# Optimization experiments

Measured on AMD Instinct MI355X. Metric: run time of the kernel, lower is better.

The kernel has to match this reference:

```python
import jax, jax.numpy as jnp
import numpy as np

HEADS = 8
DIM_HEAD = 64
QUERY_DIM = 512
CONTEXT_DIM = 768
INNER = HEADS * DIM_HEAD  # 512
SCALE = DIM_HEAD ** -0.5


def setup_inputs() -> dict:
    key = jax.random.key(0)
    ks = jax.random.split(key, 7)
    B, N, M = 4, 2048, 2048
    x = jax.random.normal(ks[0], (B, N, QUERY_DIM), dtype=jnp.float32)
    context = jax.random.normal(ks[1], (B, M, CONTEXT_DIM), dtype=jnp.float32)
    # torch Linear weights: [out_features, in_features], y = x @ W.T
    s = 0.02
    Wq = jax.random.normal(ks[2], (INNER, QUERY_DIM), dtype=jnp.float32) * s
    Wk = jax.random.normal(ks[3], (INNER, CONTEXT_DIM), dtype=jnp.float32) * s
    Wv = jax.random.normal(ks[4], (INNER, CONTEXT_DIM), dtype=jnp.float32) * s
    Wo = jax.random.normal(ks[5], (QUERY_DIM, INNER), dtype=jnp.float32) * s
    bo = jax.random.normal(ks[6], (QUERY_DIM,), dtype=jnp.float32) * s
    return {"x": x, "context": context, "Wq": Wq, "Wk": Wk, "Wv": Wv, "Wo": Wo, "bo": bo}


def reference(x, context, Wq, Wk, Wv, Wo, bo):
    b, n, _ = x.shape
    m = context.shape[1]
    h, d = HEADS, DIM_HEAD
    # Projections (bias=False for q/k/v)
    q = jnp.einsum('bnc,ec->bne', x, Wq)        # [b, n, inner]
    k = jnp.einsum('bmc,ec->bme', context, Wk)  # [b, m, inner]
    v = jnp.einsum('bmc,ec->bme', context, Wv)
    # Split heads
    q = q.reshape(b, n, h, d)
    k = k.reshape(b, m, h, d)
    v = v.reshape(b, m, h, d)
    # Scores in fp32 (original casts q,k to float), scaled by dim_head**-0.5
    sim = jnp.einsum('bihd,bjhd->bhij', q.astype(jnp.float32), k.astype(jnp.float32)) * SCALE
    attn = jax.nn.softmax(sim, axis=-1).astype(v.dtype)
    out = jnp.einsum('bhij,bjhd->bihd', attn, v).reshape(b, n, h * d)
    # Output projection with bias (dropout=0 -> identity)
    return jnp.einsum('bne,oe->bno', out, Wo) + bo
```

## Files before the change

### kernel.cpp

```cpp
#include <hip/hip_runtime.h>
#include <hip/hip_bf16.h>
#include <math.h>


typedef __bf16 bf16x8 __attribute__((ext_vector_type(8)));
typedef __bf16 bf16x4 __attribute__((ext_vector_type(4)));
typedef short s16x4 __attribute__((ext_vector_type(4)));
typedef float f32x4 __attribute__((ext_vector_type(4)));

#define QSCALE 0.18033688011112042f

__device__ __forceinline__ f32x4 mfma32(bf16x8 a, bf16x8 b, f32x4 c) {
  return __builtin_amdgcn_mfma_f32_16x16x32_bf16(a, b, c, 0, 0, 0);
}
__device__ __forceinline__ f32x4 mfma16(s16x4 a, s16x4 b, f32x4 c) {
  return __builtin_amdgcn_mfma_f32_16x16x16bf16_1k(a, b, c, 0, 0, 0);
}

__global__ __launch_bounds__(256) void cast_all(
    const float* __restrict__ x, const float* __restrict__ ctx,
    const float* __restrict__ wq, const float* __restrict__ wk,
    const float* __restrict__ wv, const float* __restrict__ wo,
    __bf16* __restrict__ xb, __bf16* __restrict__ cb,
    __bf16* __restrict__ wqb, __bf16* __restrict__ wkb,
    __bf16* __restrict__ wvb, __bf16* __restrict__ wob) {
  const int B0 = 1048576;
  const int B1 = 2621440;
  const int B2 = 2686976;
  const int B3 = 2785280;
  const int B4 = 2883584;
  const int B5 = 2949120;
  for (int i = blockIdx.x * blockDim.x + threadIdx.x; i < B5;
       i += gridDim.x * blockDim.x) {
    const float* s;
    __bf16* d;
    int off;
    if (i < B0)      { s = x;   d = xb;  off = i; }
    else if (i < B1) { s = ctx; d = cb;  off = i - B0; }
    else if (i < B2) { s = wq;  d = wqb; off = i - B1; }
    else if (i < B3) { s = wk;  d = wkb; off = i - B2; }
    else if (i < B4) { s = wv;  d = wvb; off = i - B3; }
    else             { s = wo;  d = wob; off = i - B4; }
    float4 f = ((const float4*)s)[off];
    union { __bf16 b[4]; ushort4 u; } cv;
    cv.b[0] = (__bf16)f.x; cv.b[1] = (__bf16)f.y;
    cv.b[2] = (__bf16)f.z; cv.b[3] = (__bf16)f.w;
    ((ushort4*)d)[off] = cv.u;
  }
}

template <int MODE>
__device__ __forceinline__ void gemm_body(
    const __bf16* __restrict__ A, const __bf16* __restrict__ B,
    __bf16* __restrict__ Cout, int Kd, float scale, int m0, int n0,
    __bf16 (*As)[40], __bf16 (*Bs)[40]) {
  const int t = threadIdx.x;
  const int w = t >> 6;
  const int lane = t & 63;
  const int ln = lane & 15;
  const int qd = lane >> 4;
  const int wm = (w >> 1) * 64;
  const int wn = (w & 1) * 64;

  f32x4 zero4 = {0.f, 0.f, 0.f, 0.f};
  f32x4 acc[4][4];
#pragma unroll
  for (int i = 0; i < 4; ++i)
#pragma unroll
    for (int j = 0; j < 4; ++j) acc[i][j] = zero4;

  const int r = t >> 1;
  const int c0 = (t & 1) * 16;
  const __bf16* gA = A + (size_t)(m0 + r) * Kd + c0;
  const __bf16* gB = B + (size_t)(n0 + r) * Kd + c0;

  for (int kc = 0; kc < Kd; kc += 32) {
    uint4 a0 = *(const uint4*)(gA + kc);
    uint4 a1 = *(const uint4*)(gA + kc + 8);
    uint4 b0 = *(const uint4*)(gB + kc);
    uint4 b1 = *(const uint4*)(gB + kc + 8);
    __syncthreads();
    *(uint4*)&As[r][c0] = a0;
    *(uint4*)&As[r][c0 + 8] = a1;
    *(uint4*)&Bs[r][c0] = b0;
    *(uint4*)&Bs[r][c0 + 8] = b1;
    __syncthreads();
    bf16x8 af[4], bfr[4];
#pragma unroll
    for (int i = 0; i < 4; ++i) {
      af[i] = *(const bf16x8*)&As[wm + i * 16 + ln][qd * 8];
      bfr[i] = *(const bf16x8*)&Bs[wn + i * 16 + ln][qd * 8];
    }
#pragma unroll
    for (int i = 0; i < 4; ++i)
#pragma unroll
      for (int j = 0; j < 4; ++j) {
        if (MODE == 1)
          acc[i][j] = mfma32(af[i], bfr[j], acc[i][j]);
        else
          acc[i][j] = mfma32(bfr[j], af[i], acc[i][j]);
      }
  }

#pragma unroll
  for (int i = 0; i < 4; ++i)
#pragma unroll
    for (int j = 0; j < 4; ++j) {
      if (MODE == 0) {
        const int gm = m0 + wm + i * 16 + ln;
        const int gn0 = n0 + wn + j * 16 + qd * 4;
        const int bb = gm >> 11, tok = gm & 2047;
        const int hh = gn0 >> 6, dd0 = gn0 & 63;
        bf16x4 v;
#pragma unroll
        for (int rg = 0; rg < 4; ++rg) v[rg] = (__bf16)(acc[i][j][rg] * scale);
        *(bf16x4*)(Cout + (((size_t)bb * 8 + hh) * 2048 + tok) * 64 + dd0) = v;
      } else {
        const int gm0 = m0 + wm + i * 16 + qd * 4;
        const int gn = n0 + wn + j * 16 + ln;
        const int bb = gm0 >> 11, tok0 = gm0 & 2047;
        const int hh = gn >> 6, dd = gn & 63;
        bf16x4 v;
#pragma unroll
        for (int rg = 0; rg < 4; ++rg) v[rg] = (__bf16)acc[i][j][rg];
        *(bf16x4*)(Cout + (((size_t)bb * 8 + hh) * 64 + dd) * 2048 + tok0) = v;
      }
    }
}

__global__ __launch_bounds__(256, 3) void proj_qkv(
    const __bf16* __restrict__ xb, const __bf16* __restrict__ cb,
    const __bf16* __restrict__ Wq, const __bf16* __restrict__ Wk,
    const __bf16* __restrict__ Wv, __bf16* __restrict__ Qw,
    __bf16* __restrict__ Kw, __bf16* __restrict__ Vtw) {
  __shared__ __bf16 As[128][40];
  __shared__ __bf16 Bs[128][40];
  const int m0 = blockIdx.x * 128;
  const int job = blockIdx.y >> 2;
  const int n0 = (blockIdx.y & 3) * 128;
  if (job == 0)
    gemm_body<0>(xb, Wq, Qw, 512, QSCALE, m0, n0, As, Bs);
  else if (job == 1)
    gemm_body<0>(cb, Wk, Kw, 768, 1.0f, m0, n0, As, Bs);
  else
    gemm_body<1>(cb, Wv, Vtw, 768, 1.0f, m0, n0, As, Bs);
}

__global__ __launch_bounds__(256) void gemm_out(
    const __bf16* __restrict__ A,
    const __bf16* __restrict__ B,
    float* __restrict__ C,
    const float* __restrict__ bias) {
  const int m0 = blockIdx.x * 64;
  const int n0 = blockIdx.y * 128;
  const int t = threadIdx.x;
  const int w = t >> 6;
  const int lane = t & 63;
  const int ln = lane & 15;
  const int qd = lane >> 4;
  const int wm = (w >> 1) * 32;
  const int wn = (w & 1) * 64;

  __shared__ __bf16 As[64][40];
  __shared__ __bf16 Bs[128][40];

  f32x4 zero4 = {0.f, 0.f, 0.f, 0.f};
  f32x4 acc[2][4];
#pragma unroll
  for (int i = 0; i < 2; ++i)
#pragma unroll
    for (int j = 0; j < 4; ++j) acc[i][j] = zero4;

  const int ra = t >> 2, ca = (t & 3) * 8;
  const int rb = t >> 1, cb = (t & 1) * 16;
  const __bf16* gA = A + (size_t)(m0 + ra) * 512 + ca;
  const __bf16* gB = B + (size_t)(n0 + rb) * 512 + cb;

  for (int kc = 0; kc < 512; kc += 32) {
    uint4 av = *(const uint4*)(gA + kc);
    uint4 b0 = *(const uint4*)(gB + kc);
    uint4 b1 = *(const uint4*)(gB + kc + 8);
    __syncthreads();
    *(uint4*)&As[ra][ca] = av;
    *(uint4*)&Bs[rb][cb] = b0;
    *(uint4*)&Bs[rb][cb + 8] = b1;
    __syncthreads();
    bf16x8 af[2], bfr[4];
#pragma unroll
    for (int i = 0; i < 2; ++i)
      af[i] = *(const bf16x8*)&As[wm + i * 16 + ln][qd * 8];
#pragma unroll
    for (int j = 0; j < 4; ++j)
      bfr[j] = *(const bf16x8*)&Bs[wn + j * 16 + ln][qd * 8];
#pragma unroll
    for (int i = 0; i < 2; ++i)
#pragma unroll
      for (int j = 0; j < 4; ++j)
        acc[i][j] = mfma32(bfr[j], af[i], acc[i][j]);
  }

#pragma unroll
  for (int i = 0; i < 2; ++i)
#pragma unroll
    for (int j = 0; j < 4; ++j) {
      const int gm = m0 + wm + i * 16 + ln;
      const int gn0 = n0 + wn + j * 16 + qd * 4;
      f32x4 bi = *(const f32x4*)&bias[gn0];
      f32x4 v = acc[i][j] + bi;
      *(f32x4*)&C[(size_t)gm * 512 + gn0] = v;
    }
}

__global__ __launch_bounds__(256, 3) void attn_kernel(
    const __bf16* __restrict__ Q,
    const __bf16* __restrict__ K,
    const __bf16* __restrict__ Vt,
    __bf16* __restrict__ O) {
  const int S = 2048;
  const int qt = blockIdx.x;
  const int bh = blockIdx.y;
  const int b = bh >> 3, h = bh & 7;
  const int t = threadIdx.x;
  const int w = t >> 6;
  const int lane = t & 63;
  const int ln = lane & 15;
  const int qd = lane >> 4;

  __shared__ __bf16 Qs[64][68];
  __shared__ __bf16 Ks[128][72];
  __shared__ __bf16 Vts[64][132];

  {
    const int r = t >> 2, c = (t & 3) * 16;
    const uint4* g =
        (const uint4*)(Q + ((size_t)bh * S + qt * 64 + r) * 64 + c);
    uint4 q0 = g[0], q1 = g[1];
    uint2* d = (uint2*)&Qs[r][c];
    d[0] = *(uint2*)&q0; d[1] = *((uint2*)&q0 + 1);
    d[2] = *(uint2*)&q1; d[3] = *((uint2*)&q1 + 1);
  }

  f32x4 zero4 = {0.f, 0.f, 0.f, 0.f};
  f32x4 o[4];
#pragma unroll
  for (int i = 0; i < 4; ++i) o[i] = zero4;
  float lrow = 0.f;

  const int kr = t >> 1, kc = (t & 1) * 32;
  const int vd = t >> 2, vc = (t & 3) * 32;

  for (int kt = 0; kt < 16; ++kt) {
    const uint4* gK =
        (const uint4*)(K + ((size_t)bh * S + kt * 128 + kr) * 64 + kc);
    const uint4* gV =
        (const uint4*)(Vt + ((size_t)bh * 64 + vd) * S + kt * 128 + vc);
    uint4 kv0 = gK[0], kv1 = gK[1], kv2 = gK[2], kv3 = gK[3];
    uint4 vv0 = gV[0], vv1 = gV[1], vv2 = gV[2], vv3 = gV[3];
    __syncthreads();
    {
      uint4* dK = (uint4*)&Ks[kr][kc];
      dK[0] = kv0; dK[1] = kv1; dK[2] = kv2; dK[3] = kv3;
      uint2* dV = (uint2*)&Vts[vd][vc];
      dV[0] = *(uint2*)&vv0; dV[1] = *((uint2*)&vv0 + 1);
      dV[2] = *(uint2*)&vv1; dV[3] = *((uint2*)&vv1 + 1);
      dV[4] = *(uint2*)&vv2; dV[5] = *((uint2*)&vv2 + 1);
      dV[6] = *(uint2*)&vv3; dV[7] = *((uint2*)&vv3 + 1);
    }
    __syncthreads();

    f32x4 s[8];
#pragma unroll
    for (int nt = 0; nt < 8; ++nt) s[nt] = zero4;
#pragma unroll
    for (int kst = 0; kst < 2; ++kst) {
      union { bf16x4 hh[2]; bf16x8 v; } u;
      u.hh[0] = *(const bf16x4*)&Qs[w * 16 + ln][kst * 32 + qd * 8];
      u.hh[1] = *(const bf16x4*)&Qs[w * 16 + ln][kst * 32 + qd * 8 + 4];
      bf16x8 bq = u.v;
#pragma unroll
      for (int nt = 0; nt < 8; ++nt) {
        bf16x8 ak = *(const bf16x8*)&Ks[nt * 16 + ln][kst * 32 + qd * 8];
        s[nt] = mfma32(ak, bq, s[nt]);
      }
    }

    {
      float rs = 0.f;
#pragma unroll
      for (int nt = 0; nt < 8; ++nt)
#pragma unroll
        for (int rg = 0; rg < 4; ++rg) {
          float p = exp2f(s[nt][rg]);
          s[nt][rg] = p;
          rs += p;
        }
      lrow += rs;
    }

#pragma unroll
    for (int nt = 0; nt < 8; ++nt) {
      bf16x4 c0;
#pragma unroll
      for (int rg = 0; rg < 4; ++rg) c0[rg] = (__bf16)s[nt][rg];
      s16x4 p0 = __builtin_bit_cast(s16x4, c0);
#pragma unroll
      for (int i = 0; i < 4; ++i) {
        bf16x4 av = *(const bf16x4*)&Vts[i * 16 + ln][nt * 16 + qd * 4];
        s16x4 a = __builtin_bit_cast(s16x4, av);
        o[i] = mfma16(a, p0, o[i]);
      }
    }
  }

  {
    float l = lrow;
    l += __shfl_xor(l, 16);
    l += __shfl_xor(l, 32);
    const float inv = 1.f / l;
    const int tok = qt * 64 + w * 16 + ln;
#pragma unroll
    for (int i = 0; i < 4; ++i) {
      bf16x4 v;
#pragma unroll
      for (int rg = 0; rg < 4; ++rg) v[rg] = (__bf16)(o[i][rg] * inv);
      const int col = h * 64 + i * 16 + qd * 4;
      *(bf16x4*)&O[((size_t)b * S + tok) * 512 + col] = v;
    }
  }
}

extern "C" void kernel_launch(void* const* d_in, const int* in_sizes, int n_in,
                              void* d_out, int out_size, void* d_ws,
                              size_t ws_size, hipStream_t stream) {
  const float* x = (const float*)d_in[0];
  const float* ctx = (const float*)d_in[1];
  const float* Wq = (const float*)d_in[2];
  const float* Wk = (const float*)d_in[3];
  const float* Wv = (const float*)d_in[4];
  const float* Wo = (const float*)d_in[5];
  const float* bo = (const float*)d_in[6];

  char* p = (char*)d_ws;
  __bf16* xb = (__bf16*)p;   p += (size_t)8192 * 512 * 2;
  __bf16* cb = (__bf16*)p;   p += (size_t)8192 * 768 * 2;
  __bf16* wqb = (__bf16*)p;  p += (size_t)512 * 512 * 2;
  __bf16* wkb = (__bf16*)p;  p += (size_t)512 * 768 * 2;
  __bf16* wvb = (__bf16*)p;  p += (size_t)512 * 768 * 2;
  __bf16* wob = (__bf16*)p;  p += (size_t)512 * 512 * 2;
  __bf16* Qw = (__bf16*)p;   p += (size_t)8192 * 512 * 2;
  __bf16* Kw = (__bf16*)p;   p += (size_t)8192 * 512 * 2;
  __bf16* Vtw = (__bf16*)p;  p += (size_t)8192 * 512 * 2;
  __bf16* Ow = (__bf16*)p;   p += (size_t)8192 * 512 * 2;

  cast_all<<<2880, 256, 0, stream>>>(x, ctx, Wq, Wk, Wv, Wo, xb, cb, wqb, wkb,
                                     wvb, wob);

  dim3 gp(64, 12);
  proj_qkv<<<gp, 256, 0, stream>>>(xb, cb, wqb, wkb, wvb, Qw, Kw, Vtw);

  dim3 ga(32, 32);
  attn_kernel<<<ga, 256, 0, stream>>>(Qw, Kw, Vtw, Ow);

  dim3 go(128, 4);
  gemm_out<<<go, 256, 0, stream>>>(Ow, wob, (float*)d_out, bo);
}
```

Before: 205.6 us.

## Split attention over KV halves, merge in output GEMM, use global_load_lds staging

The attention kernel now handles 128 query rows per block and splits the key range into two halves along a new grid dimension. Each half writes unnormalized partial outputs and row sums. The output GEMM sums the two partials and normalizes them while loading A, which is valid because no running max is subtracted. The QKV projection and output GEMMs also stage their B operands, and for QKV both A and B, through global_load_lds into a k-sliced LDS layout instead of register round trips. This trades extra workspace traffic for the partials against more parallel blocks and reuse of each K/V tile across more query rows.

```diff
diff --git a/kernel.cpp b/kernel.cpp
--- a/kernel.cpp
+++ b/kernel.cpp
@@ -15,6 +15,12 @@
 }
 __device__ __forceinline__ f32x4 mfma16(s16x4 a, s16x4 b, f32x4 c) {
   return __builtin_amdgcn_mfma_f32_16x16x16bf16_1k(a, b, c, 0, 0, 0);
+}
+
+__device__ __forceinline__ void glds16(const void* g, void* l) {
+  __builtin_amdgcn_global_load_lds(
+      (const __attribute__((address_space(1))) unsigned int*)g,
+      (__attribute__((address_space(3))) unsigned int*)l, 16, 0, 0);
 }
 
 __global__ __launch_bounds__(256) void cast_all(
@@ -50,10 +56,10 @@
 }
 
 template <int MODE>
-__device__ __forceinline__ void gemm_body(
+__device__ __forceinline__ void gemm_body_g(
     const __bf16* __restrict__ A, const __bf16* __restrict__ B,
     __bf16* __restrict__ Cout, int Kd, float scale, int m0, int n0,
-    __bf16 (*As)[40], __bf16 (*Bs)[40]) {
+    __bf16 (*As)[128][8], __bf16 (*Bs)[128][8]) {
   const int t = threadIdx.x;
   const int w = t >> 6;
   const int lane = t & 63;
@@ -69,27 +75,23 @@
 #pragma unroll
     for (int j = 0; j < 4; ++j) acc[i][j] = zero4;
 
-  const int r = t >> 1;
-  const int c0 = (t & 1) * 16;
-  const __bf16* gA = A + (size_t)(m0 + r) * Kd + c0;
-  const __bf16* gB = B + (size_t)(n0 + r) * Kd + c0;
+  const __bf16* gA0 = A + (size_t)(m0 + lane) * Kd + w * 8;
+  const __bf16* gA1 = A + (size_t)(m0 + 64 + lane) * Kd + w * 8;
+  const __bf16* gB0 = B + (size_t)(n0 + lane) * Kd + w * 8;
+  const __bf16* gB1 = B + (size_t)(n0 + 64 + lane) * Kd + w * 8;
 
   for (int kc = 0; kc < Kd; kc += 32) {
-    uint4 a0 = *(const uint4*)(gA + kc);
-    uint4 a1 = *(const uint4*)(gA + kc + 8);
-    uint4 b0 = *(const uint4*)(gB + kc);
-    uint4 b1 = *(const uint4*)(gB + kc + 8);
-    __syncthreads();
-    *(uint4*)&As[r][c0] = a0;
-    *(uint4*)&As[r][c0 + 8] = a1;
-    *(uint4*)&Bs[r][c0] = b0;
-    *(uint4*)&Bs[r][c0 + 8] = b1;
+    __syncthreads();
+    glds16(gA0 + kc, &As[w][0][0]);
+    glds16(gA1 + kc, &As[w][64][0]);
+    glds16(gB0 + kc, &Bs[w][0][0]);
+    glds16(gB1 + kc, &Bs[w][64][0]);
     __syncthreads();
     bf16x8 af[4], bfr[4];
 #pragma unroll
     for (int i = 0; i < 4; ++i) {
-      af[i] = *(const bf16x8*)&As[wm + i * 16 + ln][qd * 8];
-      bfr[i] = *(const bf16x8*)&Bs[wn + i * 16 + ln][qd * 8];
+      af[i] = *(const bf16x8*)&As[qd][wm + i * 16 + ln][0];
+      bfr[i] = *(const bf16x8*)&Bs[qd][wn + i * 16 + ln][0];
     }
 #pragma unroll
     for (int i = 0; i < 4; ++i)
@@ -133,21 +135,23 @@
     const __bf16* __restrict__ Wq, const __bf16* __restrict__ Wk,
     const __bf16* __restrict__ Wv, __bf16* __restrict__ Qw,
     __bf16* __restrict__ Kw, __bf16* __restrict__ Vtw) {
-  __shared__ __bf16 As[128][40];
-  __shared__ __bf16 Bs[128][40];
+  __shared__ __align__(16) __bf16 As[4][128][8];
+  __shared__ __align__(16) __bf16 Bs[4][128][8];
   const int m0 = blockIdx.x * 128;
   const int job = blockIdx.y >> 2;
   const int n0 = (blockIdx.y & 3) * 128;
   if (job == 0)
-    gemm_body<0>(xb, Wq, Qw, 512, QSCALE, m0, n0, As, Bs);
+    gemm_body_g<0>(xb, Wq, Qw, 512, QSCALE, m0, n0, As, Bs);
   else if (job == 1)
-    gemm_body<0>(cb, Wk, Kw, 768, 1.0f, m0, n0, As, Bs);
+    gemm_body_g<0>(cb, Wk, Kw, 768, 1.0f, m0, n0, As, Bs);
   else
-    gemm_body<1>(cb, Wv, Vtw, 768, 1.0f, m0, n0, As, Bs);
+    gemm_body_g<1>(cb, Wv, Vtw, 768, 1.0f, m0, n0, As, Bs);
 }
 
 __global__ __launch_bounds__(256) void gemm_out(
-    const __bf16* __restrict__ A,
+    const __bf16* __restrict__ O0,
+    const __bf16* __restrict__ O1,
+    const float* __restrict__ lbuf,
     const __bf16* __restrict__ B,
     float* __restrict__ C,
     const float* __restrict__ bias) {
@@ -161,8 +165,8 @@
   const int wm = (w >> 1) * 32;
   const int wn = (w & 1) * 64;
 
-  __shared__ __bf16 As[64][40];
-  __shared__ __bf16 Bs[128][40];
+  __shared__ __align__(16) __bf16 As[64][40];
+  __shared__ __align__(16) __bf16 Bs[4][128][8];
 
   f32x4 zero4 = {0.f, 0.f, 0.f, 0.f};
   f32x4 acc[2][4];
@@ -172,18 +176,27 @@
     for (int j = 0; j < 4; ++j) acc[i][j] = zero4;
 
   const int ra = t >> 2, ca = (t & 3) * 8;
-  const int rb = t >> 1, cb = (t & 1) * 16;
-  const __bf16* gA = A + (size_t)(m0 + ra) * 512 + ca;
-  const __bf16* gB = B + (size_t)(n0 + rb) * 512 + cb;
+  const int gm_s = m0 + ra;
+  const int bidx = gm_s >> 11, tok_s = gm_s & 2047;
+  const size_t aoff = (size_t)gm_s * 512 + ca;
+  const __bf16* gB0 = B + (size_t)(n0 + lane) * 512 + w * 8;
+  const __bf16* gB1 = B + (size_t)(n0 + 64 + lane) * 512 + w * 8;
 
   for (int kc = 0; kc < 512; kc += 32) {
-    uint4 av = *(const uint4*)(gA + kc);
-    uint4 b0 = *(const uint4*)(gB + kc);
-    uint4 b1 = *(const uint4*)(gB + kc + 8);
-    __syncthreads();
-    *(uint4*)&As[ra][ca] = av;
-    *(uint4*)&Bs[rb][cb] = b0;
-    *(uint4*)&Bs[rb][cb + 8] = b1;
+    const int hh = kc >> 6;
+    const float l0 = lbuf[((size_t)bidx * 8 + hh) * 2048 + tok_s];
+    const float l1 = lbuf[(size_t)65536 + ((size_t)bidx * 8 + hh) * 2048 + tok_s];
+    const float inv = 1.0f / (l0 + l1);
+    union { bf16x8 v; uint4 u; } u0, u1, r;
+    u0.u = *(const uint4*)(O0 + aoff + kc);
+    u1.u = *(const uint4*)(O1 + aoff + kc);
+#pragma unroll
+    for (int e = 0; e < 8; ++e)
+      r.v[e] = (__bf16)(((float)u0.v[e] + (float)u1.v[e]) * inv);
+    __syncthreads();
+    glds16(gB0 + kc, &Bs[w][0][0]);
+    glds16(gB1 + kc, &Bs[w][64][0]);
+    *(uint4*)&As[ra][ca] = r.u;
     __syncthreads();
     bf16x8 af[2], bfr[4];
 #pragma unroll
@@ -191,7 +204,7 @@
       af[i] = *(const bf16x8*)&As[wm + i * 16 + ln][qd * 8];
 #pragma unroll
     for (int j = 0; j < 4; ++j)
-      bfr[j] = *(const bf16x8*)&Bs[wn + j * 16 + ln][qd * 8];
+      bfr[j] = *(const bf16x8*)&Bs[qd][wn + j * 16 + ln][0];
 #pragma unroll
     for (int i = 0; i < 2; ++i)
 #pragma unroll
@@ -215,10 +228,12 @@
     const __bf16* __restrict__ Q,
     const __bf16* __restrict__ K,
     const __bf16* __restrict__ Vt,
-    __bf16* __restrict__ O) {
+    __bf16* __restrict__ Oh,
+    float* __restrict__ lbuf) {
   const int S = 2048;
   const int qt = blockIdx.x;
   const int bh = blockIdx.y;
+  const int sp = blockIdx.z;
   const int b = bh >> 3, h = bh & 7;
   const int t = threadIdx.x;
   const int w = t >> 6;
@@ -226,30 +241,35 @@
   const int ln = lane & 15;
   const int qd = lane >> 4;
 
-  __shared__ __bf16 Qs[64][68];
-  __shared__ __bf16 Ks[128][72];
-  __shared__ __bf16 Vts[64][132];
+  __shared__ __align__(16) __bf16 Qs[128][68];
+  __shared__ __align__(16) __bf16 Ks[128][72];
+  __shared__ __align__(16) __bf16 Vts[64][132];
 
   {
-    const int r = t >> 2, c = (t & 3) * 16;
+    const int r = t >> 1, c = (t & 1) * 32;
     const uint4* g =
-        (const uint4*)(Q + ((size_t)bh * S + qt * 64 + r) * 64 + c);
-    uint4 q0 = g[0], q1 = g[1];
+        (const uint4*)(Q + ((size_t)bh * S + qt * 128 + r) * 64 + c);
+    uint4 q0 = g[0], q1 = g[1], q2 = g[2], q3 = g[3];
     uint2* d = (uint2*)&Qs[r][c];
     d[0] = *(uint2*)&q0; d[1] = *((uint2*)&q0 + 1);
     d[2] = *(uint2*)&q1; d[3] = *((uint2*)&q1 + 1);
+    d[4] = *(uint2*)&q2; d[5] = *((uint2*)&q2 + 1);
+    d[6] = *(uint2*)&q3; d[7] = *((uint2*)&q3 + 1);
   }
 
   f32x4 zero4 = {0.f, 0.f, 0.f, 0.f};
-  f32x4 o[4];
-#pragma unroll
-  for (int i = 0; i < 4; ++i) o[i] = zero4;
-  float lrow = 0.f;
+  f32x4 o[2][4];
+#pragma unroll
+  for (int mt = 0; mt < 2; ++mt)
+#pragma unroll
+    for (int i = 0; i < 4; ++i) o[mt][i] = zero4;
+  float lrow[2] = {0.f, 0.f};
 
   const int kr = t >> 1, kc = (t & 1) * 32;
   const int vd = t >> 2, vc = (t & 3) * 32;
-
-  for (int kt = 0; kt < 16; ++kt) {
+  const int kt0 = sp * 8;
+
+  for (int kt = kt0; kt < kt0 + 8; ++kt) {
     const uint4* gK =
         (const uint4*)(K + ((size_t)bh * S + kt * 128 + kr) * 64 + kc);
     const uint4* gV =
@@ -268,63 +288,82 @@
     }
     __syncthreads();
 
-    f32x4 s[8];
-#pragma unroll
-    for (int nt = 0; nt < 8; ++nt) s[nt] = zero4;
+    f32x4 s[2][8];
+#pragma unroll
+    for (int mt = 0; mt < 2; ++mt)
+#pragma unroll
+      for (int nt = 0; nt < 8; ++nt) s[mt][nt] = zero4;
 #pragma unroll
     for (int kst = 0; kst < 2; ++kst) {
-      union { bf16x4 hh[2]; bf16x8 v; } u;
-      u.hh[0] = *(const bf16x4*)&Qs[w * 16 + ln][kst * 32 + qd * 8];
-      u.hh[1] = *(const bf16x4*)&Qs[w * 16 + ln][kst * 32 + qd * 8 + 4];
-      bf16x8 bq = u.v;
+      bf16x8 bq[2];
+#pragma unroll
+      for (int mt = 0; mt < 2; ++mt) {
+        union { bf16x4 hh[2]; bf16x8 v; } u;
+        u.hh[0] = *(const bf16x4*)&Qs[w * 32 + mt * 16 + ln][kst * 32 + qd * 8];
+        u.hh[1] =
+            *(const bf16x4*)&Qs[w * 32 + mt * 16 + ln][kst * 32 + qd * 8 + 4];
+        bq[mt] = u.v;
+      }
 #pragma unroll
       for (int nt = 0; nt < 8; ++nt) {
         bf16x8 ak = *(const bf16x8*)&Ks[nt * 16 + ln][kst * 32 + qd * 8];
-        s[nt] = mfma32(ak, bq, s[nt]);
-      }
-    }
-
-    {
+        s[0][nt] = mfma32(ak, bq[0], s[0][nt]);
+        s[1][nt] = mfma32(ak, bq[1], s[1][nt]);
+      }
+    }
+
+#pragma unroll
+    for (int mt = 0; mt < 2; ++mt) {
       float rs = 0.f;
 #pragma unroll
       for (int nt = 0; nt < 8; ++nt)
 #pragma unroll
         for (int rg = 0; rg < 4; ++rg) {
-          float p = exp2f(s[nt][rg]);
-          s[nt][rg] = p;
+          float p = exp2f(s[mt][nt][rg]);
+          s[mt][nt][rg] = p;
           rs += p;
         }
-      lrow += rs;
+      lrow[mt] += rs;
     }
 
 #pragma unroll
     for (int nt = 0; nt < 8; ++nt) {
-      bf16x4 c0;
-#pragma unroll
-      for (int rg = 0; rg < 4; ++rg) c0[rg] = (__bf16)s[nt][rg];
-      s16x4 p0 = __builtin_bit_cast(s16x4, c0);
+      s16x4 p0, p1;
+      {
+        bf16x4 c0, c1;
+#pragma unroll
+        for (int rg = 0; rg < 4; ++rg) {
+          c0[rg] = (__bf16)s[0][nt][rg];
+          c1[rg] = (__bf16)s[1][nt][rg];
+        }
+        p0 = __builtin_bit_cast(s16x4, c0);
+        p1 = __builtin_bit_cast(s16x4, c1);
+      }
 #pragma unroll
       for (int i = 0; i < 4; ++i) {
         bf16x4 av = *(const bf16x4*)&Vts[i * 16 + ln][nt * 16 + qd * 4];
         s16x4 a = __builtin_bit_cast(s16x4, av);
-        o[i] = mfma16(a, p0, o[i]);
-      }
-    }
-  }
-
-  {
-    float l = lrow;
+        o[0][i] = mfma16(a, p0, o[0][i]);
+        o[1][i] = mfma16(a, p1, o[1][i]);
+      }
+    }
+  }
+
+  __bf16* Osp = Oh + (size_t)sp * 8192 * 512;
+#pragma unroll
+  for (int mt = 0; mt < 2; ++mt) {
+    float l = lrow[mt];
     l += __shfl_xor(l, 16);
     l += __shfl_xor(l, 32);
-    const float inv = 1.f / l;
-    const int tok = qt * 64 + w * 16 + ln;
+    const int tok = qt * 128 + w * 32 + mt * 16 + ln;
+    if (qd == 0) lbuf[((size_t)sp * 32 + bh) * 2048 + tok] = l;
 #pragma unroll
     for (int i = 0; i < 4; ++i) {
       bf16x4 v;
 #pragma unroll
-      for (int rg = 0; rg < 4; ++rg) v[rg] = (__bf16)(o[i][rg] * inv);
+      for (int rg = 0; rg < 4; ++rg) v[rg] = (__bf16)o[mt][i][rg];
       const int col = h * 64 + i * 16 + qd * 4;
-      *(bf16x4*)&O[((size_t)b * S + tok) * 512 + col] = v;
+      *(bf16x4*)&Osp[((size_t)b * S + tok) * 512 + col] = v;
     }
   }
 }
@@ -350,7 +389,8 @@
   __bf16* Qw = (__bf16*)p;   p += (size_t)8192 * 512 * 2;
   __bf16* Kw = (__bf16*)p;   p += (size_t)8192 * 512 * 2;
   __bf16* Vtw = (__bf16*)p;  p += (size_t)8192 * 512 * 2;
-  __bf16* Ow = (__bf16*)p;   p += (size_t)8192 * 512 * 2;
+  __bf16* Oh = (__bf16*)p;   p += (size_t)2 * 8192 * 512 * 2;
+  float* lbuf = (float*)p;   p += (size_t)2 * 32 * 2048 * 4;
 
   cast_all<<<2880, 256, 0, stream>>>(x, ctx, Wq, Wk, Wv, Wo, xb, cb, wqb, wkb,
                                      wvb, wob);
@@ -358,9 +398,10 @@
   dim3 gp(64, 12);
   proj_qkv<<<gp, 256, 0, stream>>>(xb, cb, wqb, wkb, wvb, Qw, Kw, Vtw);
 
-  dim3 ga(32, 32);
-  attn_kernel<<<ga, 256, 0, stream>>>(Qw, Kw, Vtw, Ow);
+  dim3 ga(16, 32, 2);
+  attn_kernel<<<ga, 256, 0, stream>>>(Qw, Kw, Vtw, Oh, lbuf);
 
   dim3 go(128, 4);
-  gemm_out<<<go, 256, 0, stream>>>(Ow, wob, (float*)d_out, bo);
-}
+  gemm_out<<<go, 256, 0, stream>>>(Oh, Oh + (size_t)8192 * 512, lbuf, wob,
+                                   (float*)d_out, bo);
+}
```

Measured after the change: 217.1 us. 5.6% more time.

## Split attention over key range, merge partial outputs in output GEMM

Applied to the files above, without the earlier changes.

Attention now splits the key sequence into two halves across a third grid dimension. Each block handles 128 queries held in registers instead of 64 staged in shared memory, and writes unnormalized partial outputs plus row sums. The output-projection GEMM loads both partials, sums them, divides by the combined row sum and converts before the matmul. V^T storage is permuted so each thread fetches a 16-byte PV operand instead of two 8-byte ones. The merge is correct without a running max only because the scores are used without max subtraction. This doubles the O intermediate traffic and adds the l buffer in exchange for more reuse of K/V per block and wider loads.

```diff
diff --git a/kernel.cpp b/kernel.cpp
--- a/kernel.cpp
+++ b/kernel.cpp
@@ -118,12 +118,15 @@
       } else {
         const int gm0 = m0 + wm + i * 16 + qd * 4;
         const int gn = n0 + wn + j * 16 + ln;
-        const int bb = gm0 >> 11, tok0 = gm0 & 2047;
+        const int bb = gm0 >> 11;
+        const int tokbase = (gm0 & 2047) & ~31;
+        const int up = qd * 8 + (i & 1) * 4;
         const int hh = gn >> 6, dd = gn & 63;
         bf16x4 v;
 #pragma unroll
         for (int rg = 0; rg < 4; ++rg) v[rg] = (__bf16)acc[i][j][rg];
-        *(bf16x4*)(Cout + (((size_t)bb * 8 + hh) * 64 + dd) * 2048 + tok0) = v;
+        *(bf16x4*)(Cout + (((size_t)bb * 8 + hh) * 64 + dd) * 2048 + tokbase +
+                   up) = v;
       }
     }
 }
@@ -147,10 +150,10 @@
 }
 
 __global__ __launch_bounds__(256) void gemm_out(
-    const __bf16* __restrict__ A,
+    const __bf16* __restrict__ O0, const __bf16* __restrict__ O1,
+    const float* __restrict__ lbuf,
     const __bf16* __restrict__ B,
-    float* __restrict__ C,
-    const float* __restrict__ bias) {
+    float* __restrict__ C, const float* __restrict__ bias) {
   const int m0 = blockIdx.x * 64;
   const int n0 = blockIdx.y * 128;
   const int t = threadIdx.x;
@@ -173,15 +176,32 @@
 
   const int ra = t >> 2, ca = (t & 3) * 8;
   const int rb = t >> 1, cb = (t & 1) * 16;
-  const __bf16* gA = A + (size_t)(m0 + ra) * 512 + ca;
+  const int gm_s = m0 + ra;
+  const int bidx = gm_s >> 11, tok_s = gm_s & 2047;
+  const size_t aoff = (size_t)gm_s * 512 + ca;
   const __bf16* gB = B + (size_t)(n0 + rb) * 512 + cb;
 
+  float inv[8];
+#pragma unroll
+  for (int hh = 0; hh < 8; ++hh) {
+    const float l0 = lbuf[((size_t)bidx * 8 + hh) * 2048 + tok_s];
+    const float l1 = lbuf[65536 + ((size_t)bidx * 8 + hh) * 2048 + tok_s];
+    inv[hh] = 1.0f / (l0 + l1);
+  }
+
+#pragma unroll
   for (int kc = 0; kc < 512; kc += 32) {
-    uint4 av = *(const uint4*)(gA + kc);
+    const float iv = inv[kc >> 6];
+    union { bf16x8 v; uint4 u; } u0, u1, rr;
+    u0.u = *(const uint4*)(O0 + aoff + kc);
+    u1.u = *(const uint4*)(O1 + aoff + kc);
     uint4 b0 = *(const uint4*)(gB + kc);
     uint4 b1 = *(const uint4*)(gB + kc + 8);
-    __syncthreads();
-    *(uint4*)&As[ra][ca] = av;
+#pragma unroll
+    for (int e = 0; e < 8; ++e)
+      rr.v[e] = (__bf16)(((float)u0.v[e] + (float)u1.v[e]) * iv);
+    __syncthreads();
+    *(uint4*)&As[ra][ca] = rr.u;
     *(uint4*)&Bs[rb][cb] = b0;
     *(uint4*)&Bs[rb][cb + 8] = b1;
     __syncthreads();
@@ -211,14 +231,16 @@
     }
 }
 
-__global__ __launch_bounds__(256, 3) void attn_kernel(
+__global__ __launch_bounds__(256, 4) void attn_kernel(
     const __bf16* __restrict__ Q,
     const __bf16* __restrict__ K,
     const __bf16* __restrict__ Vt,
-    __bf16* __restrict__ O) {
+    __bf16* __restrict__ Oh,
+    float* __restrict__ lbuf) {
   const int S = 2048;
   const int qt = blockIdx.x;
   const int bh = blockIdx.y;
+  const int sp = blockIdx.z;
   const int b = bh >> 3, h = bh & 7;
   const int t = threadIdx.x;
   const int w = t >> 6;
@@ -226,30 +248,33 @@
   const int ln = lane & 15;
   const int qd = lane >> 4;
 
-  __shared__ __bf16 Qs[64][68];
-  __shared__ __bf16 Ks[128][72];
-  __shared__ __bf16 Vts[64][132];
-
+  __shared__ __align__(16) __bf16 Ks[128][72];
+  __shared__ __align__(16) __bf16 Vts[64][136];
+
+  bf16x8 bq[2][2];
   {
-    const int r = t >> 2, c = (t & 3) * 16;
-    const uint4* g =
-        (const uint4*)(Q + ((size_t)bh * S + qt * 64 + r) * 64 + c);
-    uint4 q0 = g[0], q1 = g[1];
-    uint2* d = (uint2*)&Qs[r][c];
-    d[0] = *(uint2*)&q0; d[1] = *((uint2*)&q0 + 1);
-    d[2] = *(uint2*)&q1; d[3] = *((uint2*)&q1 + 1);
+    const __bf16* qb =
+        Q + ((size_t)bh * S + qt * 128 + w * 32 + ln) * 64 + qd * 8;
+#pragma unroll
+    for (int mt = 0; mt < 2; ++mt)
+#pragma unroll
+      for (int kst = 0; kst < 2; ++kst)
+        bq[mt][kst] = *(const bf16x8*)(qb + mt * 1024 + kst * 32);
   }
 
   f32x4 zero4 = {0.f, 0.f, 0.f, 0.f};
-  f32x4 o[4];
-#pragma unroll
-  for (int i = 0; i < 4; ++i) o[i] = zero4;
-  float lrow = 0.f;
+  f32x4 o[2][4];
+#pragma unroll
+  for (int mt = 0; mt < 2; ++mt)
+#pragma unroll
+    for (int i = 0; i < 4; ++i) o[mt][i] = zero4;
+  float lrow[2] = {0.f, 0.f};
 
   const int kr = t >> 1, kc = (t & 1) * 32;
   const int vd = t >> 2, vc = (t & 3) * 32;
-
-  for (int kt = 0; kt < 16; ++kt) {
+  const int kt0 = sp * 8;
+
+  for (int kt = kt0; kt < kt0 + 8; ++kt) {
     const uint4* gK =
         (const uint4*)(K + ((size_t)bh * S + kt * 128 + kr) * 64 + kc);
     const uint4* gV =
@@ -260,71 +285,80 @@
     {
       uint4* dK = (uint4*)&Ks[kr][kc];
       dK[0] = kv0; dK[1] = kv1; dK[2] = kv2; dK[3] = kv3;
-      uint2* dV = (uint2*)&Vts[vd][vc];
-      dV[0] = *(uint2*)&vv0; dV[1] = *((uint2*)&vv0 + 1);
-      dV[2] = *(uint2*)&vv1; dV[3] = *((uint2*)&vv1 + 1);
-      dV[4] = *(uint2*)&vv2; dV[5] = *((uint2*)&vv2 + 1);
-      dV[6] = *(uint2*)&vv3; dV[7] = *((uint2*)&vv3 + 1);
-    }
-    __syncthreads();
-
-    f32x4 s[8];
-#pragma unroll
-    for (int nt = 0; nt < 8; ++nt) s[nt] = zero4;
-#pragma unroll
-    for (int kst = 0; kst < 2; ++kst) {
-      union { bf16x4 hh[2]; bf16x8 v; } u;
-      u.hh[0] = *(const bf16x4*)&Qs[w * 16 + ln][kst * 32 + qd * 8];
-      u.hh[1] = *(const bf16x4*)&Qs[w * 16 + ln][kst * 32 + qd * 8 + 4];
-      bf16x8 bq = u.v;
-#pragma unroll
-      for (int nt = 0; nt < 8; ++nt) {
-        bf16x8 ak = *(const bf16x8*)&Ks[nt * 16 + ln][kst * 32 + qd * 8];
-        s[nt] = mfma32(ak, bq, s[nt]);
+      uint4* dV = (uint4*)&Vts[vd][vc];
+      dV[0] = vv0; dV[1] = vv1; dV[2] = vv2; dV[3] = vv3;
+    }
+    __syncthreads();
+
+#pragma unroll
+    for (int c = 0; c < 4; ++c) {
+      bf16x8 av[4];
+#pragma unroll
+      for (int i = 0; i < 4; ++i)
+        av[i] = *(const bf16x8*)&Vts[i * 16 + ln][c * 32 + qd * 8];
+
+      f32x4 s[2][2];
+      s[0][0] = zero4; s[0][1] = zero4; s[1][0] = zero4; s[1][1] = zero4;
+#pragma unroll
+      for (int e = 0; e < 2; ++e) {
+        const int nt = c * 2 + e;
+#pragma unroll
+        for (int kst = 0; kst < 2; ++kst) {
+          bf16x8 ak = *(const bf16x8*)&Ks[nt * 16 + ln][kst * 32 + qd * 8];
+          s[e][0] = mfma32(ak, bq[0][kst], s[e][0]);
+          s[e][1] = mfma32(ak, bq[1][kst], s[e][1]);
+        }
       }
-    }
-
-    {
-      float rs = 0.f;
-#pragma unroll
-      for (int nt = 0; nt < 8; ++nt)
+#pragma unroll
+      for (int e = 0; e < 2; ++e)
+#pragma unroll
+        for (int mt = 0; mt < 2; ++mt) {
+          float rs = 0.f;
+#pragma unroll
+          for (int rg = 0; rg < 4; ++rg) {
+            float p = exp2f(s[e][mt][rg]);
+            s[e][mt][rg] = p;
+            rs += p;
+          }
+          lrow[mt] += rs;
+        }
+#pragma unroll
+      for (int e = 0; e < 2; ++e) {
+        bf16x4 c0, c1;
 #pragma unroll
         for (int rg = 0; rg < 4; ++rg) {
-          float p = exp2f(s[nt][rg]);
-          s[nt][rg] = p;
-          rs += p;
+          c0[rg] = (__bf16)s[e][0][rg];
+          c1[rg] = (__bf16)s[e][1][rg];
         }
-      lrow += rs;
-    }
-
-#pragma unroll
-    for (int nt = 0; nt < 8; ++nt) {
-      bf16x4 c0;
-#pragma unroll
-      for (int rg = 0; rg < 4; ++rg) c0[rg] = (__bf16)s[nt][rg];
-      s16x4 p0 = __builtin_bit_cast(s16x4, c0);
-#pragma unroll
-      for (int i = 0; i < 4; ++i) {
-        bf16x4 av = *(const bf16x4*)&Vts[i * 16 + ln][nt * 16 + qd * 4];
-        s16x4 a = __builtin_bit_cast(s16x4, av);
-        o[i] = mfma16(a, p0, o[i]);
+        s16x4 p0 = __builtin_bit_cast(s16x4, c0);
+        s16x4 p1 = __builtin_bit_cast(s16x4, c1);
+#pragma unroll
+        for (int i = 0; i < 4; ++i) {
+          union { bf16x8 v; bf16x4 hh[2]; } U;
+          U.v = av[i];
+          s16x4 a = __builtin_bit_cast(s16x4, U.hh[e]);
+          o[0][i] = mfma16(a, p0, o[0][i]);
+          o[1][i] = mfma16(a, p1, o[1][i]);
+        }
       }
     }
   }
 
-  {
-    float l = lrow;
+  __bf16* Osp = Oh + (size_t)sp * 8192 * 512;
+#pragma unroll
+  for (int mt = 0; mt < 2; ++mt) {
+    float l = lrow[mt];
     l += __shfl_xor(l, 16);
     l += __shfl_xor(l, 32);
-    const float inv = 1.f / l;
-    const int tok = qt * 64 + w * 16 + ln;
+    const int tok = qt * 128 + w * 32 + mt * 16 + ln;
+    if (qd == 0) lbuf[((size_t)sp * 32 + bh) * 2048 + tok] = l;
 #pragma unroll
     for (int i = 0; i < 4; ++i) {
       bf16x4 v;
 #pragma unroll
-      for (int rg = 0; rg < 4; ++rg) v[rg] = (__bf16)(o[i][rg] * inv);
+      for (int rg = 0; rg < 4; ++rg) v[rg] = (__bf16)o[mt][i][rg];
       const int col = h * 64 + i * 16 + qd * 4;
-      *(bf16x4*)&O[((size_t)b * S + tok) * 512 + col] = v;
+      *(bf16x4*)&Osp[((size_t)b * S + tok) * 512 + col] = v;
     }
   }
 }
@@ -350,7 +384,8 @@
   __bf16* Qw = (__bf16*)p;   p += (size_t)8192 * 512 * 2;
   __bf16* Kw = (__bf16*)p;   p += (size_t)8192 * 512 * 2;
   __bf16* Vtw = (__bf16*)p;  p += (size_t)8192 * 512 * 2;
-  __bf16* Ow = (__bf16*)p;   p += (size_t)8192 * 512 * 2;
+  __bf16* Oh = (__bf16*)p;   p += (size_t)2 * 8192 * 512 * 2;
+  float* lbuf = (float*)p;   p += (size_t)2 * 32 * 2048 * 4;
 
   cast_all<<<2880, 256, 0, stream>>>(x, ctx, Wq, Wk, Wv, Wo, xb, cb, wqb, wkb,
                                      wvb, wob);
@@ -358,9 +393,10 @@
   dim3 gp(64, 12);
   proj_qkv<<<gp, 256, 0, stream>>>(xb, cb, wqb, wkb, wvb, Qw, Kw, Vtw);
 
-  dim3 ga(32, 32);
-  attn_kernel<<<ga, 256, 0, stream>>>(Qw, Kw, Vtw, Ow);
+  dim3 ga(16, 32, 2);
+  attn_kernel<<<ga, 256, 0, stream>>>(Qw, Kw, Vtw, Oh, lbuf);
 
   dim3 go(128, 4);
-  gemm_out<<<go, 256, 0, stream>>>(Ow, wob, (float*)d_out, bo);
-}
+  gemm_out<<<go, 256, 0, stream>>>(Oh, Oh + (size_t)8192 * 512, lbuf, wob,
+                                   (float*)d_out, bo);
+}
```

Result: no change. 206.4 us (+0.4%).
